# Performance work log

Measured on AMD Instinct MI355X. Metric: run time of the kernel, lower is better.

Reference implementation:

```python
import jax, jax.numpy as jnp
import numpy as np

N_NODES = 50000
N_EDGES = 800000
D = 128
N_GRAPHS = 64


def setup_inputs() -> dict:
    key = jax.random.key(0)
    ks = jax.random.split(key, 10)
    x = jax.random.normal(ks[0], (N_NODES, D), dtype=jnp.float32)
    edge_weight = jax.random.uniform(ks[1], (N_EDGES,), dtype=jnp.float32)
    W1 = jax.random.normal(ks[2], (D, D), dtype=jnp.float32) / np.sqrt(D)
    b1 = jax.random.normal(ks[3], (D,), dtype=jnp.float32) * 0.01
    W2 = jax.random.normal(ks[4], (D, D), dtype=jnp.float32) / np.sqrt(D)
    b2 = jax.random.normal(ks[5], (D,), dtype=jnp.float32) * 0.01
    Wh = jax.random.normal(ks[6], (D, 1), dtype=jnp.float32) / np.sqrt(D)
    bh = jax.random.normal(ks[7], (1,), dtype=jnp.float32) * 0.01
    edge_index = jax.random.randint(ks[8], (2, N_EDGES), 0, N_NODES, dtype=jnp.int64)
    batch = jnp.sort(jax.random.randint(ks[9], (N_NODES,), 0, N_GRAPHS, dtype=jnp.int64))
    return {"x": x, "edge_weight": edge_weight, "W1": W1, "b1": b1,
            "W2": W2, "b2": b2, "Wh": Wh, "bh": bh,
            "edge_index": edge_index, "batch": batch}


def reference(x, edge_weight, W1, b1, W2, b2, Wh, bh, edge_index, batch):
    N = x.shape[0]
    # --- GCN normalization with self-loops (computed once; shared by layers) ---
    row, col = edge_index[0], edge_index[1]
    loop = jnp.arange(N, dtype=edge_index.dtype)
    row2 = jnp.concatenate([row, loop])   # source nodes
    col2 = jnp.concatenate([col, loop])   # target nodes
    ew2 = jnp.concatenate([edge_weight, jnp.ones((N,), dtype=x.dtype)])
    deg = jax.ops.segment_sum(ew2, col2, num_segments=N)
    dinv = jnp.where(deg > 0, jax.lax.rsqrt(deg), 0.0)
    norm = dinv[row2] * ew2 * dinv[col2]  # [E+N]

    def gcn_conv(h, W, b):
        h = h @ W                                   # [N, D_out]
        msg = norm[:, None] * h[row2]               # gather + scale, [E+N, D_out]
        return jax.ops.segment_sum(msg, col2, num_segments=N) + b

    # dropout is identity in eval mode
    h = jax.nn.relu(gcn_conv(x, W1, b1))
    h = jax.nn.relu(gcn_conv(h, W2, b2))

    # --- global mean pool over graphs ---
    counts = jax.ops.segment_sum(jnp.ones((N,), dtype=h.dtype), batch, num_segments=N_GRAPHS)
    pooled = jax.ops.segment_sum(h, batch, num_segments=N_GRAPHS)
    pooled = pooled / jnp.maximum(counts, 1.0)[:, None]
    return pooled @ Wh + bh
```

## Files before the change

### kernel.cpp

```cpp
#include <hip/hip_runtime.h>
#include <hip/hip_bf16.h>
#include <hip/hip_fp16.h>

#define N_NODES  50000
#define N_EDGES  800000
#define D        128
#define N_GRAPHS 64
#define CAP      64
#define EW_SCALE 1048576.0f
#define NB_GEMM1 391
#define NB_FILL  3125
#define NB_AGG16 3125

typedef _Float16 half8 __attribute__((ext_vector_type(8)));
typedef float   float4v __attribute__((ext_vector_type(4)));

__device__ __forceinline__ float2 h2f(unsigned int u) {
    __half2 h = *reinterpret_cast<__half2*>(&u);
    return __half22float2(h);
}
__device__ __forceinline__ unsigned int f2h(float a, float b) {
    __half2 h = __floats2half2_rn(a, b);
    return *reinterpret_cast<unsigned int*>(&h);
}
__device__ __forceinline__ float hu2f(unsigned short u) {
    __half_raw hr; hr.x = u;
    return __half2float(__half(hr));
}

__global__ __launch_bounds__(256) void fused_gemm1_fill(const float* __restrict__ X,
                                                        const float* __restrict__ W,
                                                        __half* __restrict__ Yh,
                                                        const int* __restrict__ ei,
                                                        const float* __restrict__ ew,
                                                        unsigned long long* __restrict__ packed,
                                                        unsigned int* __restrict__ bucket) {
    __shared__ float XT[32 * 128];
    __shared__ float Ws[32 * 128];

    if (blockIdx.x >= NB_GEMM1) {
        int e = (blockIdx.x - NB_GEMM1) * 256 + threadIdx.x;
        if (e >= N_EDGES) return;
        int r = ei[e];
        int c = ei[N_EDGES + e];
        float w = ew[e];
        unsigned long long add = (1ULL << 40) | (unsigned long long)(unsigned)(w * EW_SCALE + 0.5f);
        unsigned long long old = atomicAdd(&packed[c], add);
        unsigned pos = (unsigned)(old >> 40);
        if (pos < CAP) {
            unsigned short wh = __half_as_ushort(__float2half_rn(w));
            bucket[(size_t)c * CAP + pos] = (unsigned)r | ((unsigned)wh << 16);
        }
        return;
    }

    const int tid  = threadIdx.x;
    const int row0 = blockIdx.x * 128;
    const int tr = tid >> 4, tc = tid & 15;
    float acc[8][8] = {};

    for (int kt = 0; kt < 4; kt++) {
        const int kbase = kt * 32;
        {
            const float4* src = (const float4*)(W + kbase * 128);
            float4* dst = (float4*)Ws;
            for (int i = tid; i < 1024; i += 256) dst[i] = src[i];
        }
        {
            int r  = tid >> 1;
            int rr = row0 + r; if (rr >= N_NODES) rr = N_NODES - 1;
            int k0 = (tid & 1) * 16;
            const float4* src = (const float4*)(X + (size_t)rr * 128 + kbase + k0);
#pragma unroll
            for (int i = 0; i < 4; i++) {
                float4 v = src[i];
                int k = k0 + i * 4;
                XT[(k + 0) * 128 + r] = v.x;
                XT[(k + 1) * 128 + r] = v.y;
                XT[(k + 2) * 128 + r] = v.z;
                XT[(k + 3) * 128 + r] = v.w;
            }
        }
        __syncthreads();
#pragma unroll 4
        for (int k = 0; k < 32; k++) {
            float xs[8], ws[8];
            *(float4*)&xs[0] = *(const float4*)(XT + k * 128 + tr * 8);
            *(float4*)&xs[4] = *(const float4*)(XT + k * 128 + tr * 8 + 4);
            *(float4*)&ws[0] = *(const float4*)(Ws + k * 128 + tc * 8);
            *(float4*)&ws[4] = *(const float4*)(Ws + k * 128 + tc * 8 + 4);
#pragma unroll
            for (int i = 0; i < 8; i++)
#pragma unroll
                for (int j = 0; j < 8; j++)
                    acc[i][j] += xs[i] * ws[j];
        }
        __syncthreads();
    }
#pragma unroll
    for (int i = 0; i < 8; i++) {
        int r = row0 + tr * 8 + i;
        if (r < N_NODES) {
            uint4 p;
            p.x = f2h(acc[i][0], acc[i][1]);
            p.y = f2h(acc[i][2], acc[i][3]);
            p.z = f2h(acc[i][4], acc[i][5]);
            p.w = f2h(acc[i][6], acc[i][7]);
            *(uint4*)(Yh + (size_t)r * 128 + tc * 8) = p;
        }
    }
}

__global__ void dinv_gstart_kernel(const unsigned long long* __restrict__ packed,
                                   int* __restrict__ cnt, float* __restrict__ dinv,
                                   const int* __restrict__ batch, int* __restrict__ gstart) {
    int i = blockIdx.x * 256 + threadIdx.x;
    if (i >= N_NODES) return;
    unsigned long long p = packed[i];
    int c = (int)(p >> 40);
    cnt[i] = c < CAP ? c : CAP;
    float deg = 1.0f + (float)(p & 0xFFFFFFFFFFULL) * (1.0f / EW_SCALE);
    dinv[i] = rsqrtf(deg);

    int a = batch[i];
    if (i == 0) {
        for (int g = 0; g <= a; g++) gstart[g] = 0;
    } else {
        int pg = batch[i - 1];
        for (int g = pg + 1; g <= a; g++) gstart[g] = i;
    }
    if (i == N_NODES - 1) {
        for (int g = a + 1; g <= N_GRAPHS; g++) gstart[g] = N_NODES;
    }
}

__global__ __launch_bounds__(256) void agg1_gemm2_kernel(const __half* __restrict__ xw1,
                                                         const int* __restrict__ cnt,
                                                         const unsigned int* __restrict__ bucket,
                                                         const float* __restrict__ dinv,
                                                         const float* __restrict__ b1,
                                                         const float* __restrict__ W2,
                                                         __half* __restrict__ x2) {
    __shared__ _Float16 sh1[16][136];
    const int wv   = threadIdx.x >> 6;
    const int lane = threadIdx.x & 63;
    const unsigned int* xh = (const unsigned int*)xw1;
    const int node0 = blockIdx.x * 16;

    float2 bb = ((const float2*)b1)[lane];

#pragma unroll
    for (int j = 0; j < 4; j++) {
        int node = node0 + wv * 4 + j;
        float dv = dinv[node];
        int n = cnt[node];

        unsigned pk = 0u;
        if (lane < n) {
            unsigned eh = bucket[(size_t)node * CAP + lane];
            float v = hu2f((unsigned short)(eh >> 16)) * dinv[eh & 0xFFFFu];
            pk = (eh & 0xFFFFu) | ((unsigned)__half_as_ushort(__float2half_rn(v)) << 16);
        }
        int pki = (int)pk;

        float2 xs = h2f(xh[(size_t)node * 64 + lane]);
        float accx = dv * xs.x;
        float accy = dv * xs.y;

        int i = 0;
        for (; i + 3 < n; i += 4) {
            unsigned v0u = (unsigned)__shfl(pki, i);
            unsigned v1u = (unsigned)__shfl(pki, i + 1);
            unsigned v2u = (unsigned)__shfl(pki, i + 2);
            unsigned v3u = (unsigned)__shfl(pki, i + 3);
            int r0 = v0u & 0xFFFF, r1 = v1u & 0xFFFF, r2 = v2u & 0xFFFF, r3 = v3u & 0xFFFF;
            float v0 = hu2f((unsigned short)(v0u >> 16));
            float v1 = hu2f((unsigned short)(v1u >> 16));
            float v2 = hu2f((unsigned short)(v2u >> 16));
            float v3 = hu2f((unsigned short)(v3u >> 16));
            float2 f0 = h2f(xh[(size_t)r0 * 64 + lane]);
            float2 f1 = h2f(xh[(size_t)r1 * 64 + lane]);
            float2 f2 = h2f(xh[(size_t)r2 * 64 + lane]);
            float2 f3 = h2f(xh[(size_t)r3 * 64 + lane]);
            accx += v0 * f0.x + v1 * f1.x + v2 * f2.x + v3 * f3.x;
            accy += v0 * f0.y + v1 * f1.y + v2 * f2.y + v3 * f3.y;
        }
        for (; i < n; i++) {
            unsigned v0u = (unsigned)__shfl(pki, i);
            int r0 = v0u & 0xFFFF;
            float v0 = hu2f((unsigned short)(v0u >> 16));
            float2 f0 = h2f(xh[(size_t)r0 * 64 + lane]);
            accx += v0 * f0.x;
            accy += v0 * f0.y;
        }

        float hx = fmaxf(dv * accx + bb.x, 0.0f);
        float hy = fmaxf(dv * accy + bb.y, 0.0f);
        int lr = wv * 4 + j;
        sh1[lr][lane * 2]     = (_Float16)hx;
        sh1[lr][lane * 2 + 1] = (_Float16)hy;
    }
    __syncthreads();

    const int quad = lane >> 4;
    const int l16  = lane & 15;
    float4v acc0 = {}, acc1 = {};
#pragma unroll
    for (int kc = 0; kc < 4; kc++) {
        const int k0 = kc * 32;
        half8 a = *(const half8*)(&sh1[l16][k0 + quad * 8]);
        {
            const float* wp = W2 + (size_t)(k0 + quad * 8) * 128 + (wv * 2) * 16 + l16;
            half8 b;
#pragma unroll
            for (int jj = 0; jj < 8; jj++) b[jj] = (_Float16)wp[jj * 128];
            acc0 = __builtin_amdgcn_mfma_f32_16x16x32_f16(a, b, acc0, 0, 0, 0);
        }
        {
            const float* wp = W2 + (size_t)(k0 + quad * 8) * 128 + (wv * 2 + 1) * 16 + l16;
            half8 b;
#pragma unroll
            for (int jj = 0; jj < 8; jj++) b[jj] = (_Float16)wp[jj * 128];
            acc1 = __builtin_amdgcn_mfma_f32_16x16x32_f16(a, b, acc1, 0, 0, 0);
        }
    }
#pragma unroll
    for (int r = 0; r < 4; r++) {
        int row = node0 + quad * 4 + r;
        float s = dinv[row];
        x2[(size_t)row * 128 + (wv * 2) * 16 + l16]     = __float2half_rn(acc0[r] * s);
        x2[(size_t)row * 128 + (wv * 2 + 1) * 16 + l16] = __float2half_rn(acc1[r] * s);
    }
}

__global__ __launch_bounds__(256) void agg_head_kernel(const __half* __restrict__ xwh,
                                                       const int* __restrict__ cnt,
                                                       const unsigned int* __restrict__ bucket,
                                                       const float* __restrict__ dinv,
                                                       const float* __restrict__ bias,
                                                       const float* __restrict__ Wh,
                                                       float* __restrict__ nodedot) {
    int node = blockIdx.x * 4 + (threadIdx.x >> 6);
    int lane = threadIdx.x & 63;
    const unsigned int* xh = (const unsigned int*)xwh;

    float dv = dinv[node];
    int n = cnt[node];

    unsigned int ehdr = (lane < n) ? bucket[(size_t)node * CAP + lane] : 0u;
    int eh = (int)ehdr;

    float2 xs = h2f(xh[(size_t)node * 64 + lane]);
    float accx = xs.x;
    float accy = xs.y;

    int i = 0;
    for (; i + 3 < n; i += 4) {
        unsigned v0u = (unsigned)__shfl(eh, i);
        unsigned v1u = (unsigned)__shfl(eh, i + 1);
        unsigned v2u = (unsigned)__shfl(eh, i + 2);
        unsigned v3u = (unsigned)__shfl(eh, i + 3);
        int r0 = v0u & 0xFFFF, r1 = v1u & 0xFFFF, r2 = v2u & 0xFFFF, r3 = v3u & 0xFFFF;
        float v0 = hu2f((unsigned short)(v0u >> 16));
        float v1 = hu2f((unsigned short)(v1u >> 16));
        float v2 = hu2f((unsigned short)(v2u >> 16));
        float v3 = hu2f((unsigned short)(v3u >> 16));
        float2 f0 = h2f(xh[(size_t)r0 * 64 + lane]);
        float2 f1 = h2f(xh[(size_t)r1 * 64 + lane]);
        float2 f2 = h2f(xh[(size_t)r2 * 64 + lane]);
        float2 f3 = h2f(xh[(size_t)r3 * 64 + lane]);
        accx += v0 * f0.x + v1 * f1.x + v2 * f2.x + v3 * f3.x;
        accy += v0 * f0.y + v1 * f1.y + v2 * f2.y + v3 * f3.y;
    }
    for (; i < n; i++) {
        unsigned v0u = (unsigned)__shfl(eh, i);
        int r0 = v0u & 0xFFFF;
        float v0 = hu2f((unsigned short)(v0u >> 16));
        float2 f0 = h2f(xh[(size_t)r0 * 64 + lane]);
        accx += v0 * f0.x;
        accy += v0 * f0.y;
    }

    float2 b = ((const float2*)bias)[lane];
    float hx = fmaxf(dv * accx + b.x, 0.0f);
    float hy = fmaxf(dv * accy + b.y, 0.0f);
    float2 w = ((const float2*)Wh)[lane];
    float s = hx * w.x + hy * w.y;
#pragma unroll
    for (int off = 32; off > 0; off >>= 1) s += __shfl_down(s, off, 64);
    if (lane == 0) nodedot[node] = s;
}

__global__ __launch_bounds__(256) void final2_kernel(const float* __restrict__ nodedot,
                                                     const int* __restrict__ gstart,
                                                     const float* __restrict__ bh,
                                                     float* __restrict__ out) {
    __shared__ float red[256];
    int g = blockIdx.x;
    int a = gstart[g], b = gstart[g + 1];
    float s = 0.0f;
    for (int n = a + threadIdx.x; n < b; n += 256) s += nodedot[n];
    red[threadIdx.x] = s;
    __syncthreads();
#pragma unroll
    for (int off = 128; off > 0; off >>= 1) {
        if (threadIdx.x < off) red[threadIdx.x] += red[threadIdx.x + off];
        __syncthreads();
    }
    if (threadIdx.x == 0)
        out[g] = red[0] / fmaxf((float)(b - a), 1.0f) + bh[0];
}

extern "C" void kernel_launch(void* const* d_in, const int* in_sizes, int n_in,
                              void* d_out, int out_size, void* d_ws, size_t ws_size,
                              hipStream_t stream) {
    const float* x   = (const float*)d_in[0];
    const float* ew  = (const float*)d_in[1];
    const float* W1  = (const float*)d_in[2];
    const float* b1  = (const float*)d_in[3];
    const float* W2  = (const float*)d_in[4];
    const float* b2  = (const float*)d_in[5];
    const float* Wh  = (const float*)d_in[6];
    const float* bh  = (const float*)d_in[7];
    const int*   ei  = (const int*)d_in[8];
    const int*   bat = (const int*)d_in[9];
    float* out = (float*)d_out;

    char* ws = (char*)d_ws;
    __half* bufAh  = (__half*)ws;                         ws += (size_t)N_NODES * D * 2;
    __half* bufBh  = (__half*)ws;                         ws += (size_t)N_NODES * D * 2;
    unsigned int* bucket = (unsigned int*)ws;             ws += (size_t)N_NODES * CAP * 4;
    unsigned long long* packed = (unsigned long long*)ws; ws += (size_t)N_NODES * 8;
    float*  dinv    = (float*)ws;                         ws += (size_t)N_NODES * 4;
    int*    cnt     = (int*)ws;                           ws += (size_t)N_NODES * 4;
    int*    gstart  = (int*)ws;                           ws += (N_GRAPHS + 1) * 4;
    float*  nodedot = (float*)ws;                         ws += (size_t)N_NODES * 4;

    const int nb_nodes = (N_NODES + 255) / 256;
    const int nb_agg4  = N_NODES / 4;

    hipMemsetAsync(packed, 0, (size_t)N_NODES * 8, stream);

    fused_gemm1_fill<<<NB_GEMM1 + NB_FILL, 256, 0, stream>>>(x, W1, bufAh, ei, ew, packed, bucket);

    dinv_gstart_kernel<<<nb_nodes, 256, 0, stream>>>(packed, cnt, dinv, bat, gstart);

    agg1_gemm2_kernel<<<NB_AGG16, 256, 0, stream>>>(bufAh, cnt, bucket, dinv, b1, W2, bufBh);

    agg_head_kernel<<<nb_agg4, 256, 0, stream>>>(bufBh, cnt, bucket, dinv, b2, Wh, nodedot);

    final2_kernel<<<N_GRAPHS, 256, 0, stream>>>(nodedot, gstart, bh, out);
}
```

Baseline: 230.7 us.

## Drop dinv/gstart kernel: decode packed degree inline, binary-search graph bounds

Removes the separate dinv_gstart kernel. Consumers now decode count and rsqrt degree straight from the packed 64-bit accumulator, and the final pooling kernel finds each graph's node range by binary search over the sorted batch array. The agg1_gemm2 kernel moves to 512 threads with 8 waves, each aggregating 2 nodes and computing one 16-column MFMA tile instead of two. This saves a launch and the dinv/cnt arrays, at the cost of recomputing rsqrt per gather and reading 8-byte packed entries instead of 4-byte dinv values.

```diff
diff --git a/kernel.cpp b/kernel.cpp
--- a/kernel.cpp
+++ b/kernel.cpp
@@ -26,6 +26,11 @@
 __device__ __forceinline__ float hu2f(unsigned short u) {
     __half_raw hr; hr.x = u;
     return __half2float(__half(hr));
+}
+__device__ __forceinline__ void unpack_pd(unsigned long long p, int& n, float& dv) {
+    int c = (int)(p >> 40);
+    n = c < CAP ? c : CAP;
+    dv = rsqrtf(1.0f + (float)(p & 0xFFFFFFFFFFULL) * (1.0f / EW_SCALE));
 }
 
 __global__ __launch_bounds__(256) void fused_gemm1_fill(const float* __restrict__ X,
@@ -111,33 +116,9 @@
     }
 }
 
-__global__ void dinv_gstart_kernel(const unsigned long long* __restrict__ packed,
-                                   int* __restrict__ cnt, float* __restrict__ dinv,
-                                   const int* __restrict__ batch, int* __restrict__ gstart) {
-    int i = blockIdx.x * 256 + threadIdx.x;
-    if (i >= N_NODES) return;
-    unsigned long long p = packed[i];
-    int c = (int)(p >> 40);
-    cnt[i] = c < CAP ? c : CAP;
-    float deg = 1.0f + (float)(p & 0xFFFFFFFFFFULL) * (1.0f / EW_SCALE);
-    dinv[i] = rsqrtf(deg);
-
-    int a = batch[i];
-    if (i == 0) {
-        for (int g = 0; g <= a; g++) gstart[g] = 0;
-    } else {
-        int pg = batch[i - 1];
-        for (int g = pg + 1; g <= a; g++) gstart[g] = i;
-    }
-    if (i == N_NODES - 1) {
-        for (int g = a + 1; g <= N_GRAPHS; g++) gstart[g] = N_NODES;
-    }
-}
-
-__global__ __launch_bounds__(256) void agg1_gemm2_kernel(const __half* __restrict__ xw1,
-                                                         const int* __restrict__ cnt,
+__global__ __launch_bounds__(512) void agg1_gemm2_kernel(const __half* __restrict__ xw1,
+                                                         const unsigned long long* __restrict__ packed,
                                                          const unsigned int* __restrict__ bucket,
-                                                         const float* __restrict__ dinv,
                                                          const float* __restrict__ b1,
                                                          const float* __restrict__ W2,
                                                          __half* __restrict__ x2) {
@@ -150,16 +131,19 @@
     float2 bb = ((const float2*)b1)[lane];
 
 #pragma unroll
-    for (int j = 0; j < 4; j++) {
-        int node = node0 + wv * 4 + j;
-        float dv = dinv[node];
-        int n = cnt[node];
+    for (int j = 0; j < 2; j++) {
+        int node = node0 + wv * 2 + j;
+        int n; float dv;
+        unpack_pd(packed[node], n, dv);
 
         unsigned pk = 0u;
         if (lane < n) {
             unsigned eh = bucket[(size_t)node * CAP + lane];
-            float v = hu2f((unsigned short)(eh >> 16)) * dinv[eh & 0xFFFFu];
-            pk = (eh & 0xFFFFu) | ((unsigned)__half_as_ushort(__float2half_rn(v)) << 16);
+            int src = eh & 0xFFFFu;
+            int sn; float sdv;
+            unpack_pd(packed[src], sn, sdv);
+            float v = hu2f((unsigned short)(eh >> 16)) * sdv;
+            pk = (unsigned)src | ((unsigned)__half_as_ushort(__float2half_rn(v)) << 16);
         }
         int pki = (int)pk;
 
@@ -196,7 +180,7 @@
 
         float hx = fmaxf(dv * accx + bb.x, 0.0f);
         float hy = fmaxf(dv * accy + bb.y, 0.0f);
-        int lr = wv * 4 + j;
+        int lr = wv * 2 + j;
         sh1[lr][lane * 2]     = (_Float16)hx;
         sh1[lr][lane * 2 + 1] = (_Float16)hy;
     }
@@ -204,39 +188,29 @@
 
     const int quad = lane >> 4;
     const int l16  = lane & 15;
-    float4v acc0 = {}, acc1 = {};
+    float4v acc0 = {};
 #pragma unroll
     for (int kc = 0; kc < 4; kc++) {
         const int k0 = kc * 32;
         half8 a = *(const half8*)(&sh1[l16][k0 + quad * 8]);
-        {
-            const float* wp = W2 + (size_t)(k0 + quad * 8) * 128 + (wv * 2) * 16 + l16;
-            half8 b;
-#pragma unroll
-            for (int jj = 0; jj < 8; jj++) b[jj] = (_Float16)wp[jj * 128];
-            acc0 = __builtin_amdgcn_mfma_f32_16x16x32_f16(a, b, acc0, 0, 0, 0);
-        }
-        {
-            const float* wp = W2 + (size_t)(k0 + quad * 8) * 128 + (wv * 2 + 1) * 16 + l16;
-            half8 b;
-#pragma unroll
-            for (int jj = 0; jj < 8; jj++) b[jj] = (_Float16)wp[jj * 128];
-            acc1 = __builtin_amdgcn_mfma_f32_16x16x32_f16(a, b, acc1, 0, 0, 0);
-        }
+        const float* wp = W2 + (size_t)(k0 + quad * 8) * 128 + wv * 16 + l16;
+        half8 b;
+#pragma unroll
+        for (int jj = 0; jj < 8; jj++) b[jj] = (_Float16)wp[jj * 128];
+        acc0 = __builtin_amdgcn_mfma_f32_16x16x32_f16(a, b, acc0, 0, 0, 0);
     }
 #pragma unroll
     for (int r = 0; r < 4; r++) {
         int row = node0 + quad * 4 + r;
-        float s = dinv[row];
-        x2[(size_t)row * 128 + (wv * 2) * 16 + l16]     = __float2half_rn(acc0[r] * s);
-        x2[(size_t)row * 128 + (wv * 2 + 1) * 16 + l16] = __float2half_rn(acc1[r] * s);
+        int rn; float s;
+        unpack_pd(packed[row], rn, s);
+        x2[(size_t)row * 128 + wv * 16 + l16] = __float2half_rn(acc0[r] * s);
     }
 }
 
 __global__ __launch_bounds__(256) void agg_head_kernel(const __half* __restrict__ xwh,
-                                                       const int* __restrict__ cnt,
+                                                       const unsigned long long* __restrict__ packed,
                                                        const unsigned int* __restrict__ bucket,
-                                                       const float* __restrict__ dinv,
                                                        const float* __restrict__ bias,
                                                        const float* __restrict__ Wh,
                                                        float* __restrict__ nodedot) {
@@ -244,8 +218,8 @@
     int lane = threadIdx.x & 63;
     const unsigned int* xh = (const unsigned int*)xwh;
 
-    float dv = dinv[node];
-    int n = cnt[node];
+    int n; float dv;
+    unpack_pd(packed[node], n, dv);
 
     unsigned int ehdr = (lane < n) ? bucket[(size_t)node * CAP + lane] : 0u;
     int eh = (int)ehdr;
@@ -292,12 +266,18 @@
 }
 
 __global__ __launch_bounds__(256) void final2_kernel(const float* __restrict__ nodedot,
-                                                     const int* __restrict__ gstart,
+                                                     const int* __restrict__ batch,
                                                      const float* __restrict__ bh,
                                                      float* __restrict__ out) {
     __shared__ float red[256];
     int g = blockIdx.x;
-    int a = gstart[g], b = gstart[g + 1];
+    int lo = 0, hi = N_NODES;
+    while (lo < hi) { int mid = (lo + hi) >> 1; if (batch[mid] < g) lo = mid + 1; else hi = mid; }
+    int a = lo;
+    hi = N_NODES;
+    while (lo < hi) { int mid = (lo + hi) >> 1; if (batch[mid] < g + 1) lo = mid + 1; else hi = mid; }
+    int b = lo;
+
     float s = 0.0f;
     for (int n = a + threadIdx.x; n < b; n += 256) s += nodedot[n];
     red[threadIdx.x] = s;
@@ -331,23 +311,17 @@
     __half* bufBh  = (__half*)ws;                         ws += (size_t)N_NODES * D * 2;
     unsigned int* bucket = (unsigned int*)ws;             ws += (size_t)N_NODES * CAP * 4;
     unsigned long long* packed = (unsigned long long*)ws; ws += (size_t)N_NODES * 8;
-    float*  dinv    = (float*)ws;                         ws += (size_t)N_NODES * 4;
-    int*    cnt     = (int*)ws;                           ws += (size_t)N_NODES * 4;
-    int*    gstart  = (int*)ws;                           ws += (N_GRAPHS + 1) * 4;
     float*  nodedot = (float*)ws;                         ws += (size_t)N_NODES * 4;
 
-    const int nb_nodes = (N_NODES + 255) / 256;
-    const int nb_agg4  = N_NODES / 4;
+    const int nb_agg4 = N_NODES / 4;
 
     hipMemsetAsync(packed, 0, (size_t)N_NODES * 8, stream);
 
     fused_gemm1_fill<<<NB_GEMM1 + NB_FILL, 256, 0, stream>>>(x, W1, bufAh, ei, ew, packed, bucket);
 
-    dinv_gstart_kernel<<<nb_nodes, 256, 0, stream>>>(packed, cnt, dinv, bat, gstart);
-
-    agg1_gemm2_kernel<<<NB_AGG16, 256, 0, stream>>>(bufAh, cnt, bucket, dinv, b1, W2, bufBh);
-
-    agg_head_kernel<<<nb_agg4, 256, 0, stream>>>(bufBh, cnt, bucket, dinv, b2, Wh, nodedot);
-
-    final2_kernel<<<N_GRAPHS, 256, 0, stream>>>(nodedot, gstart, bh, out);
-}
+    agg1_gemm2_kernel<<<NB_AGG16, 512, 0, stream>>>(bufAh, packed, bucket, b1, W2, bufBh);
+
+    agg_head_kernel<<<nb_agg4, 256, 0, stream>>>(bufBh, packed, bucket, b2, Wh, nodedot);
+
+    final2_kernel<<<N_GRAPHS, 256, 0, stream>>>(nodedot, bat, bh, out);
+}
```

New measurement: 225.9 us. 2.1% less time.
